# Kernel tuning notes

Measured on AMD Instinct MI355X. Metric: run time of the kernel, lower is better.

The kernel has to match this reference:

```python
import jax, jax.numpy as jnp
import numpy as np

NB_CLASSES = 4
MRG = 0.05
ALPHA = 32.0
CL_W = 0.05
Z_PRUNE = 0.3
EPS = 1e-12


def _proxy_anchor(X, labels, valid, P):
    # X: [N, D] flattened span-pair features; labels: [N] int; valid: [N] float mask; P: [C, D]
    Xn = X / jnp.maximum(jnp.linalg.norm(X, axis=1, keepdims=True), EPS)
    Pn = P / jnp.maximum(jnp.linalg.norm(P, axis=1, keepdims=True), EPS)
    cos = Xn @ Pn.T  # [N, C]
    onehot = jax.nn.one_hot(labels, NB_CLASSES, dtype=cos.dtype)
    p_hot = onehot * valid[:, None]
    n_hot = (1.0 - onehot) * valid[:, None]
    pos_exp = jnp.exp(-ALPHA * (cos - MRG))
    neg_exp = jnp.exp(ALPHA * (cos + MRG))
    P_sim_sum = (p_hot * pos_exp).sum(axis=0)  # [C]
    N_sim_sum = (n_hot * neg_exp).sum(axis=0)  # [C]
    num_valid = jnp.maximum((p_hot.sum(axis=0) > 0).sum(), 1).astype(cos.dtype)
    pos_term = jnp.log1p(P_sim_sum).sum() / num_valid
    neg_term = jnp.log1p(N_sim_sum).sum() / NB_CLASSES
    return pos_term + neg_term


def _cl_loss(table, labels, attention_mask, P):
    B, L = table.shape[0], table.shape[1]
    lens = attention_mask.sum(axis=1)  # [B]
    idx = jnp.arange(L)
    rv = (idx[None, :] >= 1) & (idx[None, :] < (lens[:, None] - 1))  # [B, L]
    valid = (rv[:, :, None] & rv[:, None, :]).reshape(B, L * L).astype(table.dtype)
    X = table.reshape(B, L * L, -1)
    lab = labels.reshape(B, L * L)
    per_sample = jax.vmap(lambda x, l, v: _proxy_anchor(x, l, v, P))(X, lab, valid)
    return (CL_W * per_sample).mean()


def _span_pruning(pred, z, attention_mask):
    B = attention_mask.shape[0]
    mask_len = attention_mask.sum(axis=1) - 2
    length = (mask_len.astype(jnp.float32) * z).astype(jnp.int32)
    length = jnp.maximum(length, 10)
    length = jnp.minimum(length, mask_len * mask_len)
    pred_sort = -jnp.sort(-pred.reshape(B, -1), axis=1)  # descending
    topkth = pred_sort[jnp.arange(B), length - 1]
    return pred >= topkth[:, None, None]


def setup_inputs() -> dict:
    key = jax.random.key(0)
    ks = jax.random.split(key, 8)
    B, L, D = 4, 128, 768
    return {
        "table_edge": jax.random.normal(ks[0], (B, L, L, D), dtype=jnp.float32),
        "table_senti": jax.random.normal(ks[1], (B, L, L, D), dtype=jnp.float32),
        "attention_mask": jnp.ones((B, L), dtype=jnp.int32),
        "table_labels_S": jax.random.randint(ks[2], (B, L, L), 0, 2, dtype=jnp.int32),
        "table_labels_E": jax.random.randint(ks[3], (B, L, L), 0, 2, dtype=jnp.int32),
        "labels_edge": jax.random.randint(ks[4], (B, L, L), 0, 4, dtype=jnp.int32),
        "labels_senti": jax.random.randint(ks[5], (B, L, L), 0, 4, dtype=jnp.int32),
        "proxies_edge": jax.random.normal(ks[6], (4, D), dtype=jnp.float32),
        "proxies_senti": jax.random.normal(ks[7], (4, D), dtype=jnp.float32),
        "w_S": jax.random.normal(jax.random.fold_in(key, 10), (D,), dtype=jnp.float32) * 0.02,
        "b_S": jnp.zeros((1,), dtype=jnp.float32),
        "w_E": jax.random.normal(jax.random.fold_in(key, 11), (D,), dtype=jnp.float32) * 0.02,
        "b_E": jnp.zeros((1,), dtype=jnp.float32),
        "ID": 1,
        "epoch": 1,
    }


def reference(table_edge, table_senti, attention_mask, table_labels_S, table_labels_E,
              labels_edge, labels_senti, proxies_edge, proxies_senti,
              w_S, b_S, w_E, b_E, ID, epoch):
    cl_edge = _cl_loss(table_edge, labels_edge, attention_mask, proxies_edge)
    cl_senti = _cl_loss(table_senti, labels_senti, attention_mask, proxies_senti)

    logits_S = jnp.einsum('blmd,d->blm', table_edge, w_S) + b_S[0]
    logits_E = jnp.einsum('blmd,d->blm', table_edge, w_E) + b_E[0]

    weight = (table_labels_S >= 0).astype(logits_S.dtype)
    tS = table_labels_S.astype(logits_S.dtype)
    tE = table_labels_E.astype(logits_E.dtype)
    # BCEWithLogits: softplus(x) - x*t, weighted, mean over all elements
    loss_S = (weight * (jax.nn.softplus(logits_S) - logits_S * tS)).mean()
    loss_E = (weight * (jax.nn.softplus(logits_E) - logits_E * tE)).mean()

    S_pred = jax.nn.sigmoid(logits_S) * weight
    E_pred = jax.nn.sigmoid(logits_E) * weight
    pred_S = _span_pruning(S_pred, Z_PRUNE, attention_mask)
    pred_E = _span_pruning(E_pred, Z_PRUNE, attention_mask)

    return cl_edge, cl_senti, loss_S, loss_E, pred_S, pred_E
```

## Files before the change

kernel.cpp:

```cpp
#include <hip/hip_runtime.h>
#include <math.h>

#define LSEQ 128
#define NLL 16384
#define NBATCH 4
#define DIM 768
#define NB 4
#define ALPHA_C 32.0f
#define MRG_C 0.05f
#define CLW_C 0.05f
#define BPB 128
#define KS 24

__device__ __forceinline__ float wave_reduce_f(float v) {
#pragma unroll
    for (int s = 1; s < 64; s <<= 1) v += __shfl_xor(v, s);
    return v;
}

__device__ __forceinline__ float dot4(float4 a, float4 b) {
    return a.x*b.x + a.y*b.y + a.z*b.z + a.w*b.w;
}

template<bool EDGE>
__device__ __forceinline__ void kloop4(const float* __restrict__ rp,
                                       const float* __restrict__ wlds, int sub,
                                       float (&xx)[4], float (&d0)[4], float (&d1)[4],
                                       float (&d2)[4], float (&d3)[4],
                                       float (&dS)[4], float (&dE)[4])
{
#pragma unroll 2
    for (int k = 0; k < KS; ++k) {
        const int off = k*32 + sub*4;
        float4 x[4];
#pragma unroll
        for (int rr = 0; rr < 4; ++rr)
            x[rr] = *reinterpret_cast<const float4*>(rp + (size_t)rr*DIM + off);
        const float4 w0 = *reinterpret_cast<const float4*>(&wlds[0*DIM + off]);
        const float4 w1 = *reinterpret_cast<const float4*>(&wlds[1*DIM + off]);
        const float4 w2 = *reinterpret_cast<const float4*>(&wlds[2*DIM + off]);
        const float4 w3 = *reinterpret_cast<const float4*>(&wlds[3*DIM + off]);
        float4 w4, w5;
        if constexpr (EDGE) {
            w4 = *reinterpret_cast<const float4*>(&wlds[4*DIM + off]);
            w5 = *reinterpret_cast<const float4*>(&wlds[5*DIM + off]);
        }
#pragma unroll
        for (int rr = 0; rr < 4; ++rr) {
            xx[rr] += dot4(x[rr], x[rr]);
            d0[rr] += dot4(x[rr], w0);
            d1[rr] += dot4(x[rr], w1);
            d2[rr] += dot4(x[rr], w2);
            d3[rr] += dot4(x[rr], w3);
            if constexpr (EDGE) { dS[rr] += dot4(x[rr], w4); dE[rr] += dot4(x[rr], w5); }
        }
    }
}

__global__ __launch_bounds__(256, 4)
void fused_pass(const float* __restrict__ tabE, const float* __restrict__ tabS,
                const int* __restrict__ labE, const int* __restrict__ labSen,
                const int* __restrict__ attn,
                const float* __restrict__ proxE, const float* __restrict__ proxSen,
                const float* __restrict__ wS, const float* __restrict__ bS,
                const float* __restrict__ wE, const float* __restrict__ bE,
                const int* __restrict__ tlabS, const int* __restrict__ tlabE,
                float* __restrict__ pS, float* __restrict__ pE,
                float* __restrict__ partE, float* __restrict__ partSen)
{
    __shared__ float wlds[6*DIM];
    __shared__ float red[4][7*32];
    __shared__ float sacc[4][14];

    const int tid = threadIdx.x, wib = tid >> 6, lane = tid & 63;
    const int tbl = blockIdx.x & 1;
    const int g = blockIdx.x >> 1;
    const int row0 = g << 7;
    const int b = g >> 7;
    const bool EDGE = (tbl == 0);

    const float* table = EDGE ? tabE : tabS;
    const float* prox  = EDGE ? proxE : proxSen;
    const int NW = EDGE ? 6 : 4;

    for (int i2 = tid; i2 < NW*192; i2 += 256) {
        const int v = i2 / 192, e = (i2 % 192) * 4;
        const float* src = (v < 4) ? (prox + v*DIM + e) : ((v == 4) ? (wS + e) : (wE + e));
        *reinterpret_cast<float4*>(&wlds[v*DIM + e]) = *reinterpret_cast<const float4*>(src);
    }
    __syncthreads();

    int lens_i = attn[b*LSEQ + lane] + attn[b*LSEQ + 64 + lane];
#pragma unroll
    for (int s = 1; s < 64; s <<= 1) lens_i += __shfl_xor(lens_i, s);
    float pinv[NB];
#pragma unroll
    for (int c = 0; c < NB; ++c) {
        float s2 = 0.f;
#pragma unroll
        for (int t = 0; t < 12; ++t) { const float w = wlds[c*DIM + t*64 + lane]; s2 += w*w; }
        s2 = wave_reduce_f(s2);
        pinv[c] = 1.0f / fmaxf(sqrtf(s2), 1e-12f);
    }

    const int rgrp = lane >> 3, sub = lane & 7;
    const int rbase = row0 + wib*32 + rgrp*4;
    const float* rp = table + (size_t)rbase * DIM;

    float xx[4]={0,0,0,0}, d0[4]={0,0,0,0}, d1[4]={0,0,0,0}, d2[4]={0,0,0,0},
          d3[4]={0,0,0,0}, dS[4]={0,0,0,0}, dE[4]={0,0,0,0};
    if (EDGE) kloop4<true >(rp, wlds, sub, xx, d0, d1, d2, d3, dS, dE);
    else      kloop4<false>(rp, wlds, sub, xx, d0, d1, d2, d3, dS, dE);

#pragma unroll
    for (int s = 1; s < 8; s <<= 1) {
#pragma unroll
        for (int rr = 0; rr < 4; ++rr) {
            xx[rr] += __shfl_xor(xx[rr], s);
            d0[rr] += __shfl_xor(d0[rr], s); d1[rr] += __shfl_xor(d1[rr], s);
            d2[rr] += __shfl_xor(d2[rr], s); d3[rr] += __shfl_xor(d3[rr], s);
        }
        if (EDGE) {
#pragma unroll
            for (int rr = 0; rr < 4; ++rr) {
                dS[rr] += __shfl_xor(dS[rr], s); dE[rr] += __shfl_xor(dE[rr], s);
            }
        }
    }
    if (sub == 0) {
        float* rw = red[wib];
        const int rb = rgrp*4;
        *reinterpret_cast<float4*>(&rw[0*32+rb]) = make_float4(xx[0],xx[1],xx[2],xx[3]);
        *reinterpret_cast<float4*>(&rw[1*32+rb]) = make_float4(d0[0],d0[1],d0[2],d0[3]);
        *reinterpret_cast<float4*>(&rw[2*32+rb]) = make_float4(d1[0],d1[1],d1[2],d1[3]);
        *reinterpret_cast<float4*>(&rw[3*32+rb]) = make_float4(d2[0],d2[1],d2[2],d2[3]);
        *reinterpret_cast<float4*>(&rw[4*32+rb]) = make_float4(d3[0],d3[1],d3[2],d3[3]);
        if (EDGE) {
            *reinterpret_cast<float4*>(&rw[5*32+rb]) = make_float4(dS[0],dS[1],dS[2],dS[3]);
            *reinterpret_cast<float4*>(&rw[6*32+rb]) = make_float4(dE[0],dE[1],dE[2],dE[3]);
        }
    }
    asm volatile("s_waitcnt lgkmcnt(0)" ::: "memory");

    float Pa[NB]={0,0,0,0}, Na[NB]={0,0,0,0}, Ca[NB]={0,0,0,0};
    float sBS = 0.f, sBE = 0.f;
    if (lane < 32) {
        const int r = row0 + wib*32 + lane;
        const float* rw = red[wib];
        const float xxv = rw[lane];
        float dd[NB] = { rw[32+lane], rw[64+lane], rw[96+lane], rw[128+lane] };
        const float xinv = 1.0f / fmaxf(sqrtf(xxv), 1e-12f);
        const int i = r & (NLL - 1);
        const int l = i >> 7, m = i & (LSEQ - 1);
        const bool valid = (l >= 1) && (l < lens_i - 1) && (m >= 1) && (m < lens_i - 1);
        const int lab = (EDGE ? labE : labSen)[r];
        if (valid) {
#pragma unroll
            for (int c = 0; c < NB; ++c) {
                const float cs = dd[c] * xinv * pinv[c];
                if (lab == c) { Pa[c] = expf(-ALPHA_C * (cs - MRG_C)); Ca[c] = 1.f; }
                else          { Na[c] = expf( ALPHA_C * (cs + MRG_C)); }
            }
        }
        if (EDGE) {
            const float dSl = rw[160+lane], dEl = rw[192+lane];
            const float xSl = dSl + bS[0], xEl = dEl + bE[0];
            const int ls = tlabS[r], le = tlabE[r];
            const float w = (ls >= 0) ? 1.f : 0.f;
            const float spS = fmaxf(xSl, 0.f) + log1pf(expf(-fabsf(xSl)));
            const float spE = fmaxf(xEl, 0.f) + log1pf(expf(-fabsf(xEl)));
            sBS = w * (spS - xSl * (float)ls);
            sBE = w * (spE - xEl * (float)le);
            pS[r] = w / (1.f + expf(-xSl));
            pE[r] = w / (1.f + expf(-xEl));
        }
    }
#pragma unroll
    for (int c = 0; c < NB; ++c) {
        Pa[c] = wave_reduce_f(Pa[c]); Na[c] = wave_reduce_f(Na[c]); Ca[c] = wave_reduce_f(Ca[c]);
    }
    sBS = wave_reduce_f(sBS); sBE = wave_reduce_f(sBE);
    if (lane == 0) {
        float* sp = sacc[wib];
#pragma unroll
        for (int c = 0; c < NB; ++c) { sp[c] = Pa[c]; sp[4+c] = Na[c]; sp[8+c] = Ca[c]; }
        sp[12] = sBS; sp[13] = sBE;
    }
    __syncthreads();
    if (tid < 14) {
        const float s = sacc[0][tid] + sacc[1][tid] + sacc[2][tid] + sacc[3][tid];
        float* pp = EDGE ? partE : partSen;
        const int blk = g & (BPB - 1);
        pp[(b * 14 + tid) * BPB + blk] = s;
    }
}

__global__ __launch_bounds__(1024)
void tail_k(const float* __restrict__ pS, const float* __restrict__ pE,
            const int* __restrict__ attn,
            const float* __restrict__ partE, const float* __restrict__ partS,
            float* __restrict__ out)
{
    __shared__ unsigned sh[NLL];
    __shared__ int csum[16];
    __shared__ float gg[56];
    const int tid = threadIdx.x, wave = tid >> 6, lane = tid & 63;

    if (blockIdx.x >= 8) {
        const int tbl = blockIdx.x - 8;
        const float* part = (tbl == 0) ? partE : partS;
        for (int grp = wave; grp < 56; grp += 16) {
            float s = 0.f;
#pragma unroll
            for (int j = lane; j < BPB; j += 64) s += part[grp*BPB + j];
            s = wave_reduce_f(s);
            if (lane == 0) gg[grp] = s;
        }
        __syncthreads();
        if (tid == 0) {
            float tot = 0.f;
            for (int b = 0; b < NBATCH; ++b) {
                const float* G = gg + b * 14;
                int nv = 0;
                for (int c = 0; c < NB; ++c) nv += (G[8+c] > 0.f) ? 1 : 0;
                const float nvf = (float)((nv > 1) ? nv : 1);
                float pos = 0.f, neg = 0.f;
                for (int c = 0; c < NB; ++c) { pos += log1pf(G[c]); neg += log1pf(G[4+c]); }
                tot += pos / nvf + neg * 0.25f;
            }
            out[tbl] = CLW_C * tot * 0.25f;
            if (tbl == 0) {
                float bs = 0.f, be = 0.f;
                for (int b = 0; b < NBATCH; ++b) { bs += gg[b*14 + 12]; be += gg[b*14 + 13]; }
                out[2] = bs * (1.0f / 65536.0f);
                out[3] = be * (1.0f / 65536.0f);
            }
        }
        return;
    }

    const int a = blockIdx.x >> 2;
    const int b = blockIdx.x & 3;
    const float* p = (a ? pE : pS) + (size_t)b * NLL;
    float* o = out + 4 + (size_t)a * (NBATCH * NLL) + (size_t)b * NLL;

    int asum = attn[b*LSEQ + lane] + attn[b*LSEQ + 64 + lane];
#pragma unroll
    for (int s = 1; s < 64; s <<= 1) asum += __shfl_xor(asum, s);
    const int mask_len = asum - 2;
    int k = (int)((float)mask_len * 0.3f);
    k = (k > 10) ? k : 10;
    const int ml2 = mask_len * mask_len;
    k = (k < ml2) ? k : ml2;

    for (int j = tid; j < NLL; j += 1024) sh[j] = __float_as_uint(p[j]);
    __syncthreads();

    unsigned lo = 0u, hi = 0xFFFFFFFFu;
    for (int it = 0; it < 32; ++it) {
        if (lo >= hi) break;
        const unsigned span = hi - lo;
        const unsigned mid = lo + (span >> 1) + (span & 1u);
        int c = 0;
        for (int j = tid; j < NLL; j += 1024) c += (sh[j] >= mid) ? 1 : 0;
#pragma unroll
        for (int s = 1; s < 64; s <<= 1) c += __shfl_xor(c, s);
        if (lane == 0) csum[wave] = c;
        __syncthreads();
        int tot = 0;
#pragma unroll
        for (int w = 0; w < 16; ++w) tot += csum[w];
        if (tot >= k) lo = mid; else hi = mid - 1u;
        __syncthreads();
    }

    for (int j = tid; j < NLL; j += 1024) o[j] = (sh[j] >= lo) ? 1.0f : 0.0f;
}

extern "C" void kernel_launch(void* const* d_in, const int* in_sizes, int n_in,
                              void* d_out, int out_size, void* d_ws, size_t ws_size,
                              hipStream_t stream)
{
    const float* table_edge  = (const float*)d_in[0];
    const float* table_senti = (const float*)d_in[1];
    const int*   attn        = (const int*)d_in[2];
    const int*   tlabS       = (const int*)d_in[3];
    const int*   tlabE       = (const int*)d_in[4];
    const int*   lab_edge    = (const int*)d_in[5];
    const int*   lab_senti   = (const int*)d_in[6];
    const float* prox_edge   = (const float*)d_in[7];
    const float* prox_senti  = (const float*)d_in[8];
    const float* w_S         = (const float*)d_in[9];
    const float* b_S         = (const float*)d_in[10];
    const float* w_E         = (const float*)d_in[11];
    const float* b_E         = (const float*)d_in[12];

    float* out   = (float*)d_out;
    float* ws    = (float*)d_ws;
    float* pS    = ws;
    float* pE    = ws + 65536;
    float* partE = ws + 131072;
    float* partS = partE + 7168;

    fused_pass<<<1024, 256, 0, stream>>>(table_edge, table_senti,
        lab_edge, lab_senti, attn, prox_edge, prox_senti,
        w_S, b_S, w_E, b_E, tlabS, tlabE, pS, pE, partE, partS);
    tail_k<<<10, 1024, 0, stream>>>(pS, pE, attn, partE, partS, out);
}
```

Baseline: 126.2 us.

## Process one row per wave with register-held proxies and full-wave shuffle reduction

Restructures the streaming pass so each wave handles 8 rows, with all 64 lanes covering one 768-wide row (3 float4 per lane). Proxy and linear weights now sit in registers instead of LDS, and the block grid grows fourfold (32 rows per block) with matching partial-sum buffers. The aim is better memory-level parallelism and less LDS traffic, at the price of a long 6-step shuffle reduction of up to 7 values per row. The row loop is not unrolled, which may leave few loads in flight. The tail kernel must handle 512 partials per batch.

```diff
diff --git a/kernel.cpp b/kernel.cpp
--- a/kernel.cpp
+++ b/kernel.cpp
@@ -9,8 +9,7 @@
 #define ALPHA_C 32.0f
 #define MRG_C 0.05f
 #define CLW_C 0.05f
-#define BPB 128
-#define KS 24
+#define BPB 512
 
 __device__ __forceinline__ float wave_reduce_f(float v) {
 #pragma unroll
@@ -20,41 +19,6 @@
 
 __device__ __forceinline__ float dot4(float4 a, float4 b) {
     return a.x*b.x + a.y*b.y + a.z*b.z + a.w*b.w;
-}
-
-template<bool EDGE>
-__device__ __forceinline__ void kloop4(const float* __restrict__ rp,
-                                       const float* __restrict__ wlds, int sub,
-                                       float (&xx)[4], float (&d0)[4], float (&d1)[4],
-                                       float (&d2)[4], float (&d3)[4],
-                                       float (&dS)[4], float (&dE)[4])
-{
-#pragma unroll 2
-    for (int k = 0; k < KS; ++k) {
-        const int off = k*32 + sub*4;
-        float4 x[4];
-#pragma unroll
-        for (int rr = 0; rr < 4; ++rr)
-            x[rr] = *reinterpret_cast<const float4*>(rp + (size_t)rr*DIM + off);
-        const float4 w0 = *reinterpret_cast<const float4*>(&wlds[0*DIM + off]);
-        const float4 w1 = *reinterpret_cast<const float4*>(&wlds[1*DIM + off]);
-        const float4 w2 = *reinterpret_cast<const float4*>(&wlds[2*DIM + off]);
-        const float4 w3 = *reinterpret_cast<const float4*>(&wlds[3*DIM + off]);
-        float4 w4, w5;
-        if constexpr (EDGE) {
-            w4 = *reinterpret_cast<const float4*>(&wlds[4*DIM + off]);
-            w5 = *reinterpret_cast<const float4*>(&wlds[5*DIM + off]);
-        }
-#pragma unroll
-        for (int rr = 0; rr < 4; ++rr) {
-            xx[rr] += dot4(x[rr], x[rr]);
-            d0[rr] += dot4(x[rr], w0);
-            d1[rr] += dot4(x[rr], w1);
-            d2[rr] += dot4(x[rr], w2);
-            d3[rr] += dot4(x[rr], w3);
-            if constexpr (EDGE) { dS[rr] += dot4(x[rr], w4); dE[rr] += dot4(x[rr], w5); }
-        }
-    }
 }
 
 __global__ __launch_bounds__(256, 4)
@@ -68,93 +32,89 @@
                 float* __restrict__ pS, float* __restrict__ pE,
                 float* __restrict__ partE, float* __restrict__ partSen)
 {
-    __shared__ float wlds[6*DIM];
-    __shared__ float red[4][7*32];
     __shared__ float sacc[4][14];
 
     const int tid = threadIdx.x, wib = tid >> 6, lane = tid & 63;
     const int tbl = blockIdx.x & 1;
     const int g = blockIdx.x >> 1;
-    const int row0 = g << 7;
-    const int b = g >> 7;
+    const int b = g >> 9;
+    const int wave_row0 = g*32 + wib*8;
     const bool EDGE = (tbl == 0);
 
-    const float* table = EDGE ? tabE : tabS;
-    const float* prox  = EDGE ? proxE : proxSen;
-    const int NW = EDGE ? 6 : 4;
-
-    for (int i2 = tid; i2 < NW*192; i2 += 256) {
-        const int v = i2 / 192, e = (i2 % 192) * 4;
-        const float* src = (v < 4) ? (prox + v*DIM + e) : ((v == 4) ? (wS + e) : (wE + e));
-        *reinterpret_cast<float4*>(&wlds[v*DIM + e]) = *reinterpret_cast<const float4*>(src);
-    }
-    __syncthreads();
+    const float* table  = EDGE ? tabE : tabS;
+    const float* prox   = EDGE ? proxE : proxSen;
+    const int*   labels = EDGE ? labE : labSen;
 
     int lens_i = attn[b*LSEQ + lane] + attn[b*LSEQ + 64 + lane];
 #pragma unroll
     for (int s = 1; s < 64; s <<= 1) lens_i += __shfl_xor(lens_i, s);
+
+    float4 px[NB][3];
     float pinv[NB];
 #pragma unroll
     for (int c = 0; c < NB; ++c) {
         float s2 = 0.f;
 #pragma unroll
-        for (int t = 0; t < 12; ++t) { const float w = wlds[c*DIM + t*64 + lane]; s2 += w*w; }
+        for (int t = 0; t < 3; ++t) {
+            px[c][t] = *reinterpret_cast<const float4*>(prox + c*DIM + t*256 + lane*4);
+            s2 += dot4(px[c][t], px[c][t]);
+        }
         s2 = wave_reduce_f(s2);
         pinv[c] = 1.0f / fmaxf(sqrtf(s2), 1e-12f);
     }
-
-    const int rgrp = lane >> 3, sub = lane & 7;
-    const int rbase = row0 + wib*32 + rgrp*4;
-    const float* rp = table + (size_t)rbase * DIM;
-
-    float xx[4]={0,0,0,0}, d0[4]={0,0,0,0}, d1[4]={0,0,0,0}, d2[4]={0,0,0,0},
-          d3[4]={0,0,0,0}, dS[4]={0,0,0,0}, dE[4]={0,0,0,0};
-    if (EDGE) kloop4<true >(rp, wlds, sub, xx, d0, d1, d2, d3, dS, dE);
-    else      kloop4<false>(rp, wlds, sub, xx, d0, d1, d2, d3, dS, dE);
-
-#pragma unroll
-    for (int s = 1; s < 8; s <<= 1) {
-#pragma unroll
-        for (int rr = 0; rr < 4; ++rr) {
-            xx[rr] += __shfl_xor(xx[rr], s);
-            d0[rr] += __shfl_xor(d0[rr], s); d1[rr] += __shfl_xor(d1[rr], s);
-            d2[rr] += __shfl_xor(d2[rr], s); d3[rr] += __shfl_xor(d3[rr], s);
-        }
+    float4 vs[3], ve[3];
+    if (EDGE) {
+#pragma unroll
+        for (int t = 0; t < 3; ++t) {
+            vs[t] = *reinterpret_cast<const float4*>(wS + t*256 + lane*4);
+            ve[t] = *reinterpret_cast<const float4*>(wE + t*256 + lane*4);
+        }
+    }
+
+    float s_xx=0, s_d0=0, s_d1=0, s_d2=0, s_d3=0, s_dS=0, s_dE=0;
+
+    const float* rowbase = table + (size_t)wave_row0 * DIM + lane*4;
+
+#pragma unroll 1
+    for (int rr = 0; rr < 8; ++rr) {
+        const float* xb = rowbase + rr*DIM;
+        const float4 x0 = *reinterpret_cast<const float4*>(xb);
+        const float4 x1 = *reinterpret_cast<const float4*>(xb + 256);
+        const float4 x2 = *reinterpret_cast<const float4*>(xb + 512);
+        float xx = dot4(x0,x0) + dot4(x1,x1) + dot4(x2,x2);
+        float d0 = dot4(x0,px[0][0]) + dot4(x1,px[0][1]) + dot4(x2,px[0][2]);
+        float d1 = dot4(x0,px[1][0]) + dot4(x1,px[1][1]) + dot4(x2,px[1][2]);
+        float d2 = dot4(x0,px[2][0]) + dot4(x1,px[2][1]) + dot4(x2,px[2][2]);
+        float d3 = dot4(x0,px[3][0]) + dot4(x1,px[3][1]) + dot4(x2,px[3][2]);
+        float dS = 0.f, dE = 0.f;
         if (EDGE) {
-#pragma unroll
-            for (int rr = 0; rr < 4; ++rr) {
-                dS[rr] += __shfl_xor(dS[rr], s); dE[rr] += __shfl_xor(dE[rr], s);
-            }
-        }
-    }
-    if (sub == 0) {
-        float* rw = red[wib];
-        const int rb = rgrp*4;
-        *reinterpret_cast<float4*>(&rw[0*32+rb]) = make_float4(xx[0],xx[1],xx[2],xx[3]);
-        *reinterpret_cast<float4*>(&rw[1*32+rb]) = make_float4(d0[0],d0[1],d0[2],d0[3]);
-        *reinterpret_cast<float4*>(&rw[2*32+rb]) = make_float4(d1[0],d1[1],d1[2],d1[3]);
-        *reinterpret_cast<float4*>(&rw[3*32+rb]) = make_float4(d2[0],d2[1],d2[2],d2[3]);
-        *reinterpret_cast<float4*>(&rw[4*32+rb]) = make_float4(d3[0],d3[1],d3[2],d3[3]);
-        if (EDGE) {
-            *reinterpret_cast<float4*>(&rw[5*32+rb]) = make_float4(dS[0],dS[1],dS[2],dS[3]);
-            *reinterpret_cast<float4*>(&rw[6*32+rb]) = make_float4(dE[0],dE[1],dE[2],dE[3]);
-        }
-    }
-    asm volatile("s_waitcnt lgkmcnt(0)" ::: "memory");
+            dS = dot4(x0,vs[0]) + dot4(x1,vs[1]) + dot4(x2,vs[2]);
+            dE = dot4(x0,ve[0]) + dot4(x1,ve[1]) + dot4(x2,ve[2]);
+        }
+#pragma unroll
+        for (int s = 1; s < 64; s <<= 1) {
+            xx += __shfl_xor(xx, s);
+            d0 += __shfl_xor(d0, s); d1 += __shfl_xor(d1, s);
+            d2 += __shfl_xor(d2, s); d3 += __shfl_xor(d3, s);
+            if (EDGE) { dS += __shfl_xor(dS, s); dE += __shfl_xor(dE, s); }
+        }
+        if (lane == rr) {
+            s_xx = xx; s_d0 = d0; s_d1 = d1; s_d2 = d2; s_d3 = d3;
+            s_dS = dS; s_dE = dE;
+        }
+    }
 
     float Pa[NB]={0,0,0,0}, Na[NB]={0,0,0,0}, Ca[NB]={0,0,0,0};
     float sBS = 0.f, sBE = 0.f;
-    if (lane < 32) {
-        const int r = row0 + wib*32 + lane;
-        const float* rw = red[wib];
-        const float xxv = rw[lane];
-        float dd[NB] = { rw[32+lane], rw[64+lane], rw[96+lane], rw[128+lane] };
-        const float xinv = 1.0f / fmaxf(sqrtf(xxv), 1e-12f);
+    if (lane < 8) {
+        const int r = wave_row0 + lane;
         const int i = r & (NLL - 1);
         const int l = i >> 7, m = i & (LSEQ - 1);
         const bool valid = (l >= 1) && (l < lens_i - 1) && (m >= 1) && (m < lens_i - 1);
-        const int lab = (EDGE ? labE : labSen)[r];
+        const float xinv = 1.0f / fmaxf(sqrtf(s_xx), 1e-12f);
         if (valid) {
+            const int lab = labels[r];
+            float dd[NB] = { s_d0, s_d1, s_d2, s_d3 };
 #pragma unroll
             for (int c = 0; c < NB; ++c) {
                 const float cs = dd[c] * xinv * pinv[c];
@@ -163,8 +123,7 @@
             }
         }
         if (EDGE) {
-            const float dSl = rw[160+lane], dEl = rw[192+lane];
-            const float xSl = dSl + bS[0], xEl = dEl + bE[0];
+            const float xSl = s_dS + bS[0], xEl = s_dE + bE[0];
             const int ls = tlabS[r], le = tlabE[r];
             const float w = (ls >= 0) ? 1.f : 0.f;
             const float spS = fmaxf(xSl, 0.f) + log1pf(expf(-fabsf(xSl)));
@@ -176,10 +135,15 @@
         }
     }
 #pragma unroll
-    for (int c = 0; c < NB; ++c) {
-        Pa[c] = wave_reduce_f(Pa[c]); Na[c] = wave_reduce_f(Na[c]); Ca[c] = wave_reduce_f(Ca[c]);
-    }
-    sBS = wave_reduce_f(sBS); sBE = wave_reduce_f(sBE);
+    for (int s = 1; s < 8; s <<= 1) {
+#pragma unroll
+        for (int c = 0; c < NB; ++c) {
+            Pa[c] += __shfl_xor(Pa[c], s);
+            Na[c] += __shfl_xor(Na[c], s);
+            Ca[c] += __shfl_xor(Ca[c], s);
+        }
+        sBS += __shfl_xor(sBS, s); sBE += __shfl_xor(sBE, s);
+    }
     if (lane == 0) {
         float* sp = sacc[wib];
 #pragma unroll
@@ -300,9 +264,9 @@
     float* pS    = ws;
     float* pE    = ws + 65536;
     float* partE = ws + 131072;
-    float* partS = partE + 7168;
-
-    fused_pass<<<1024, 256, 0, stream>>>(table_edge, table_senti,
+    float* partS = partE + 28672;
+
+    fused_pass<<<4096, 256, 0, stream>>>(table_edge, table_senti,
         lab_edge, lab_senti, attn, prox_edge, prox_senti,
         w_S, b_S, w_E, b_E, tlabS, tlabE, pS, pE, partE, partS);
     tail_k<<<10, 1024, 0, stream>>>(pS, pE, attn, partE, partS, out);
```

Result: slower. 145.5 us (+15.3%).
